# Kernel optimization log

Measured on AMD Instinct MI355X. Metric: run time of the kernel, lower is better.

## Reference

```python
import jax, jax.numpy as jnp
import numpy as np

B, C, F = 262144, 64, 256
N_ITERS = 8


def setup_inputs() -> dict:
    key = jax.random.key(0)
    ks = jax.random.split(key, 8)
    s = lambda fan_in: 1.0 / np.sqrt(fan_in)
    return {
        "y": jax.random.normal(ks[0], (B, C), jnp.float32),
        "log_det_jacobians": jnp.zeros((B,), jnp.float32),
        "v": jax.random.normal(ks[1], (B, 1, C), jnp.float32),
        "W1": jax.random.normal(ks[2], (F, C), jnp.float32) * s(C),
        "b1": jnp.zeros((F,), jnp.float32),
        "W2": jax.random.normal(ks[3], (F, F), jnp.float32) * s(F),
        "b2": jnp.zeros((F,), jnp.float32),
        "W3": jax.random.normal(ks[4], (C, F), jnp.float32) * s(F),
        "b3": jnp.zeros((C,), jnp.float32),
    }


def reference(y, log_det_jacobians, v, W1, b1, W2, b2, W3, b3):
    def mlp(t):
        h = jax.nn.elu(t)
        h = jax.nn.elu(h @ W1.T + b1)
        h = jax.nn.elu(h @ W2.T + b2)
        return h @ W3.T + b3  # [B, C]

    g_y, vjp_fn = jax.vjp(mlp, y)
    v0 = v[:, 0, :]  # n_samples = 1
    w = v0
    log_det = jnp.zeros((y.shape[0],), y.dtype)
    for k in range(1, N_ITERS + 1):
        w = vjp_fn(w)[0]              # w <- w @ J, J = dg/dy
        inner = jnp.einsum('bd,bd->b', w, v0)
        # torch code: add when (k+1) % 2 == 0 (k odd), subtract when k even
        log_det = log_det + (inner / k if (k + 1) % 2 == 0 else -inner / k)

    z = y + g_y
    return z, log_det_jacobians + log_det
```

## Files before the change

### kernel.cpp

```cpp
#include <hip/hip_runtime.h>

#define BN 262144

typedef short bf16x8 __attribute__((ext_vector_type(8)));
typedef float f32x4 __attribute__((ext_vector_type(4)));

#define MFMA16(a,b,c) __builtin_amdgcn_mfma_f32_16x16x32_bf16((a),(b),(c),0,0,0)

__device__ __forceinline__ unsigned short f2bf(float f) {
  union { float f; unsigned int u; } x; x.f = f;
  unsigned int u = x.u + 0x7fffu + ((x.u >> 16) & 1u);
  return (unsigned short)(u >> 16);
}
__device__ __forceinline__ float bf2f(unsigned int h) {
  union { unsigned int u; float f; } x; x.u = h << 16;
  return x.f;
}
__device__ __forceinline__ unsigned short tbf(float f) {
  union { float f; unsigned int u; } x; x.f = f;
  return (unsigned short)(x.u >> 16);
}

#define O_R1 0
#define O_R2 16384
#define O_R3 81920
#define O_R4 98304
#define O_R5 114688
#define O_R6 180224
#define N_WS 196608

__global__ void invres_prep(const float* __restrict__ W1, const float* __restrict__ W2,
                            const float* __restrict__ W3, unsigned short* __restrict__ wsb) {
  int idx = blockIdx.x * 256 + threadIdx.x;
  if (idx >= N_WS) return;
  int j = idx & 7;
  int lane = (idx >> 3) & 63;
  int nn = lane & 15, kn = (lane >> 4) * 8 + j;
  float val;
  if (idx < O_R2) {
    int g = idx >> 9; int s = g & 1; int ct = g >> 1;
    val = W1[(ct * 16 + nn) * 64 + (s * 32 + kn)];
  } else if (idx < O_R3) {
    int g = (idx - O_R2) >> 9; int s = g & 7; int ct = g >> 3;
    val = W2[(ct * 16 + nn) * 256 + (s * 32 + kn)];
  } else if (idx < O_R4) {
    int g = (idx - O_R3) >> 9; int s = g & 7; int ct = g >> 3;
    val = W3[(ct * 16 + nn) * 256 + (s * 32 + kn)];
  } else if (idx < O_R5) {
    int g = (idx - O_R4) >> 9; int s = g & 1; int ct = g >> 1;
    val = W3[(s * 32 + kn) * 256 + (ct * 16 + nn)];
  } else if (idx < O_R6) {
    int g = (idx - O_R5) >> 9; int s = g & 7; int ct = g >> 3;
    val = W2[(s * 32 + kn) * 256 + (ct * 16 + nn)];
  } else {
    int g = (idx - O_R6) >> 9; int s = g & 7; int ct = g >> 3;
    val = W1[(s * 32 + kn) * 64 + (ct * 16 + nn)];
  }
  wsb[idx] = f2bf(val);
}

#define L_PB  16384
#define L_WB  32768
#define L_LDP 36864
#define L_SIZE 37376

__global__ void __launch_bounds__(512, 4)
invres_main(const float* __restrict__ y, const float* __restrict__ ldj,
            const float* __restrict__ v, const float* __restrict__ b1,
            const float* __restrict__ b2, const float* __restrict__ b3,
            const unsigned short* __restrict__ wsb, float* __restrict__ out) {
  extern __shared__ char smem[];
  char* PA = smem;
  char* PB = smem + L_PB;
  char* WB = smem + L_WB;
  float* ldp = (float*)(smem + L_LDP);

  const int tid = threadIdx.x;
  const int lane = tid & 63;
  const int wid = tid >> 6;
  const int l15 = lane & 15, g16 = lane >> 4;
  const int ct0 = wid * 2;
  const int mh = wid >> 2;
  const int ctn = wid & 3;
  const int r0 = blockIdx.x * 32;

  const bf16x8* R1 = (const bf16x8*)(wsb + O_R1);
  const bf16x8* R2 = (const bf16x8*)(wsb + O_R2);
  const bf16x8* R3 = (const bf16x8*)(wsb + O_R3);
  const bf16x8* R4 = (const bf16x8*)(wsb + O_R4);
  const bf16x8* R5 = (const bf16x8*)(wsb + O_R5);
  const bf16x8* R6 = (const bf16x8*)(wsb + O_R6);

  auto ldsA = [&](const char* buf, int mm, int s) -> bf16x8 {
    int row = mm * 16 + l15;
    unsigned byte = ((unsigned)(s * 64 + g16 * 16)) ^ ((unsigned)(row & 7) << 4);
    return *(const bf16x8*)(buf + row * 512 + byte);
  };
  auto dstoreW = [&](char* buf, int mm, int cc, int r, float val) {
    int row = mm * 16 + g16 * 4 + r;
    int col = (ct0 + cc) * 16 + l15;
    *(unsigned short*)(buf + row * 512 + (((unsigned)(col * 2)) ^ ((unsigned)(row & 7) << 4))) = tbf(val);
  };
  auto gA = [&](const float* p, int mm, int s, bool elu) -> bf16x8 {
    const float* q = p + (size_t)(r0 + mm * 16 + l15) * 64 + s * 32 + g16 * 8;
    f32x4 a = __builtin_nontemporal_load((const f32x4*)q);
    f32x4 b = __builtin_nontemporal_load((const f32x4*)(q + 4));
    float xv[8] = {a[0], a[1], a[2], a[3], b[0], b[1], b[2], b[3]};
    bf16x8 f;
#pragma unroll
    for (int i = 0; i < 8; i++) {
      float x = xv[i];
      if (elu) x = x > 0.f ? x : (__expf(x) - 1.f);
      f[i] = (short)f2bf(x);
    }
    return f;
  };

  float bb1[2], bb2[2];
#pragma unroll
  for (int cc = 0; cc < 2; cc++) {
    bb1[cc] = b1[(ct0 + cc) * 16 + l15];
    bb2[cc] = b2[(ct0 + cc) * 16 + l15];
  }
  const float bb3 = b3[ctn * 16 + l15];

  unsigned d1p[8], d2p[8], d0p[2], v0p[2];
  float ldacc[4] = {0.f, 0.f, 0.f, 0.f};

  {
    f32x4 acc[2][2] = {};
#pragma unroll
    for (int s = 0; s < 2; s++) {
      bf16x8 a0 = gA(y, 0, s, true);
      bf16x8 a1 = gA(y, 1, s, true);
#pragma unroll
      for (int cc = 0; cc < 2; cc++) {
        bf16x8 B = R1[((ct0 + cc) * 2 + s) * 64 + lane];
        acc[0][cc] = MFMA16(a0, B, acc[0][cc]);
        acc[1][cc] = MFMA16(a1, B, acc[1][cc]);
      }
    }
#pragma unroll
    for (int mm = 0; mm < 2; mm++)
#pragma unroll
      for (int cc = 0; cc < 2; cc++)
#pragma unroll
        for (int r = 0; r < 4; r++) {
          float a = acc[mm][cc][r] + bb1[cc];
          float e = __expf(a);
          float h = a > 0.f ? a : (e - 1.f);
          unsigned dd = f2bf(a > 0.f ? 1.f : e);
          dstoreW(PA, mm, cc, r, h);
          int idx = (mm * 2 + cc) * 2 + (r >> 1);
          d1p[idx] = (r & 1) ? (d1p[idx] | (dd << 16)) : dd;
        }
  }
  __syncthreads();

  {
    f32x4 acc[2][2] = {};
#pragma unroll 1
    for (int s = 0; s < 8; s++) {
      bf16x8 a0 = ldsA(PA, 0, s);
      bf16x8 a1 = ldsA(PA, 1, s);
#pragma unroll
      for (int cc = 0; cc < 2; cc++) {
        bf16x8 B = R2[((ct0 + cc) * 8 + s) * 64 + lane];
        acc[0][cc] = MFMA16(a0, B, acc[0][cc]);
        acc[1][cc] = MFMA16(a1, B, acc[1][cc]);
      }
    }
#pragma unroll
    for (int mm = 0; mm < 2; mm++)
#pragma unroll
      for (int cc = 0; cc < 2; cc++)
#pragma unroll
        for (int r = 0; r < 4; r++) {
          float a = acc[mm][cc][r] + bb2[cc];
          float e = __expf(a);
          float h = a > 0.f ? a : (e - 1.f);
          unsigned dd = f2bf(a > 0.f ? 1.f : e);
          dstoreW(PB, mm, cc, r, h);
          int idx = (mm * 2 + cc) * 2 + (r >> 1);
          d2p[idx] = (r & 1) ? (d2p[idx] | (dd << 16)) : dd;
        }
  }
  __syncthreads();

  {
    f32x4 acc = {};
#pragma unroll 1
    for (int s = 0; s < 8; s++)
      acc = MFMA16(ldsA(PB, mh, s), R3[(ctn * 8 + s) * 64 + lane], acc);
#pragma unroll
    for (int r = 0; r < 4; r++) {
      int row = r0 + mh * 16 + g16 * 4 + r;
      int col = ctn * 16 + l15;
      size_t off = (size_t)row * 64 + col;
      float yv = __builtin_nontemporal_load(y + off);
      __builtin_nontemporal_store(yv + acc[r] + bb3, out + off);
      unsigned dd = f2bf(yv > 0.f ? 1.f : __expf(yv));
      unsigned vv = f2bf(__builtin_nontemporal_load(v + off));
      d0p[r >> 1] = (r & 1) ? (d0p[r >> 1] | (dd << 16)) : dd;
      v0p[r >> 1] = (r & 1) ? (v0p[r >> 1] | (vv << 16)) : vv;
    }
  }

  {
    f32x4 acc[2][2] = {};
#pragma unroll
    for (int s = 0; s < 2; s++) {
      bf16x8 a0 = gA(v, 0, s, false);
      bf16x8 a1 = gA(v, 1, s, false);
#pragma unroll
      for (int cc = 0; cc < 2; cc++) {
        bf16x8 B = R4[((ct0 + cc) * 2 + s) * 64 + lane];
        acc[0][cc] = MFMA16(a0, B, acc[0][cc]);
        acc[1][cc] = MFMA16(a1, B, acc[1][cc]);
      }
    }
#pragma unroll
    for (int mm = 0; mm < 2; mm++)
#pragma unroll
      for (int cc = 0; cc < 2; cc++)
#pragma unroll
        for (int r = 0; r < 4; r++) {
          int idx = (mm * 2 + cc) * 2 + (r >> 1);
          float u = acc[mm][cc][r] * bf2f((d2p[idx] >> ((r & 1) * 16)) & 0xffffu);
          dstoreW(PA, mm, cc, r, u);
        }
  }
  __syncthreads();

  for (int k = 1; k <= 8; ++k) {
    {
      f32x4 acc[2][2] = {};
#pragma unroll 1
      for (int s = 0; s < 8; s++) {
        bf16x8 a0 = ldsA(PA, 0, s);
        bf16x8 a1 = ldsA(PA, 1, s);
#pragma unroll
        for (int cc = 0; cc < 2; cc++) {
          bf16x8 B = R5[((ct0 + cc) * 8 + s) * 64 + lane];
          acc[0][cc] = MFMA16(a0, B, acc[0][cc]);
          acc[1][cc] = MFMA16(a1, B, acc[1][cc]);
        }
      }
#pragma unroll
      for (int mm = 0; mm < 2; mm++)
#pragma unroll
        for (int cc = 0; cc < 2; cc++)
#pragma unroll
          for (int r = 0; r < 4; r++) {
            int idx = (mm * 2 + cc) * 2 + (r >> 1);
            float u = acc[mm][cc][r] * bf2f((d1p[idx] >> ((r & 1) * 16)) & 0xffffu);
            dstoreW(PB, mm, cc, r, u);
          }
    }
    __syncthreads();

    {
      float coef = (k & 1) ? (1.f / (float)k) : (-1.f / (float)k);
      f32x4 acc = {};
#pragma unroll 1
      for (int s = 0; s < 8; s++)
        acc = MFMA16(ldsA(PB, mh, s), R6[(ctn * 8 + s) * 64 + lane], acc);
#pragma unroll
      for (int r = 0; r < 4; r++) {
        float wv = acc[r] * bf2f((d0p[r >> 1] >> ((r & 1) * 16)) & 0xffffu);
        ldacc[r] += coef * wv * bf2f((v0p[r >> 1] >> ((r & 1) * 16)) & 0xffffu);
        if (k < 8) {
          int row = mh * 16 + g16 * 4 + r;
          int col = ctn * 16 + l15;
          *(unsigned short*)(WB + row * 128 + (((unsigned)(col * 2)) ^ ((unsigned)(row & 7) << 4))) = tbf(wv);
        }
      }
    }
    if (k < 8) {
      __syncthreads();
      f32x4 acc[2][2] = {};
#pragma unroll
      for (int s = 0; s < 2; s++) {
        bf16x8 a0, a1;
#pragma unroll
        for (int mm = 0; mm < 2; mm++) {
          int row = mm * 16 + l15;
          unsigned byte = ((unsigned)(s * 64 + g16 * 16)) ^ ((unsigned)(row & 7) << 4);
          bf16x8 a = *(const bf16x8*)(WB + row * 128 + byte);
          if (mm == 0) a0 = a; else a1 = a;
        }
#pragma unroll
        for (int cc = 0; cc < 2; cc++) {
          bf16x8 B = R4[((ct0 + cc) * 2 + s) * 64 + lane];
          acc[0][cc] = MFMA16(a0, B, acc[0][cc]);
          acc[1][cc] = MFMA16(a1, B, acc[1][cc]);
        }
      }
#pragma unroll
      for (int mm = 0; mm < 2; mm++)
#pragma unroll
        for (int cc = 0; cc < 2; cc++)
#pragma unroll
          for (int r = 0; r < 4; r++) {
            int idx = (mm * 2 + cc) * 2 + (r >> 1);
            float u = acc[mm][cc][r] * bf2f((d2p[idx] >> ((r & 1) * 16)) & 0xffffu);
            dstoreW(PA, mm, cc, r, u);
          }
      __syncthreads();
    }
  }

#pragma unroll
  for (int r = 0; r < 4; r++) {
    float s = ldacc[r];
    s += __shfl_xor(s, 1);
    s += __shfl_xor(s, 2);
    s += __shfl_xor(s, 4);
    s += __shfl_xor(s, 8);
    ldacc[r] = s;
  }
  if (l15 == 0) {
#pragma unroll
    for (int r = 0; r < 4; r++) {
      int row = mh * 16 + g16 * 4 + r;
      ldp[row * 4 + ctn] = ldacc[r];
    }
  }
  __syncthreads();
  if (tid < 32) {
    float s = ldp[tid * 4] + ldp[tid * 4 + 1] + ldp[tid * 4 + 2] + ldp[tid * 4 + 3];
    int gb = r0 + tid;
    __builtin_nontemporal_store(ldj[gb] + s, out + (size_t)BN * 64 + gb);
  }
}

extern "C" void kernel_launch(void* const* d_in, const int* in_sizes, int n_in,
                              void* d_out, int out_size, void* d_ws, size_t ws_size,
                              hipStream_t stream) {
  const float* y   = (const float*)d_in[0];
  const float* ldj = (const float*)d_in[1];
  const float* v   = (const float*)d_in[2];
  const float* W1  = (const float*)d_in[3];
  const float* b1  = (const float*)d_in[4];
  const float* W2  = (const float*)d_in[5];
  const float* b2  = (const float*)d_in[6];
  const float* W3  = (const float*)d_in[7];
  const float* b3  = (const float*)d_in[8];
  unsigned short* wsb = (unsigned short*)d_ws;
  float* out = (float*)d_out;

  (void)hipFuncSetAttribute(reinterpret_cast<const void*>(&invres_main),
                            hipFuncAttributeMaxDynamicSharedMemorySize, L_SIZE);

  invres_prep<<<N_WS / 256, 256, 0, stream>>>(W1, W2, W3, wsb);
  invres_main<<<BN / 32, 512, L_SIZE, stream>>>(y, ldj, v, b1, b2, b3, wsb, out);
}
```

Before: 841.7 us.

## Double rows per block to reuse each weight fragment across four M-tiles

Each block now processes 64 batch rows instead of 32, so every wave applies each B weight fragment loaded from global/L2 to four 16-row tiles instead of two. This halves weight fetches per row and doubles MFMA work per load. In exchange, LDS per block roughly doubles to about 74 KB and register pressure rises from larger accumulator and derivative arrays, which may lower occupancy below the launch-bounds target of 4 blocks per CU.

```diff
diff --git a/kernel.cpp b/kernel.cpp
--- a/kernel.cpp
+++ b/kernel.cpp
@@ -59,10 +59,10 @@
   wsb[idx] = f2bf(val);
 }
 
-#define L_PB  16384
-#define L_WB  32768
-#define L_LDP 36864
-#define L_SIZE 37376
+#define L_PB  32768
+#define L_WB  65536
+#define L_LDP 73728
+#define L_SIZE 74752
 
 __global__ void __launch_bounds__(512, 4)
 invres_main(const float* __restrict__ y, const float* __restrict__ ldj,
@@ -80,9 +80,9 @@
   const int wid = tid >> 6;
   const int l15 = lane & 15, g16 = lane >> 4;
   const int ct0 = wid * 2;
-  const int mh = wid >> 2;
+  const int mq = (wid >> 2) * 2;
   const int ctn = wid & 3;
-  const int r0 = blockIdx.x * 32;
+  const int r0 = blockIdx.x * 64;
 
   const bf16x8* R1 = (const bf16x8*)(wsb + O_R1);
   const bf16x8* R2 = (const bf16x8*)(wsb + O_R2);
@@ -124,24 +124,26 @@
   }
   const float bb3 = b3[ctn * 16 + l15];
 
-  unsigned d1p[8], d2p[8], d0p[2], v0p[2];
-  float ldacc[4] = {0.f, 0.f, 0.f, 0.f};
+  unsigned d1p[16], d2p[16], d0p[4], v0p[4];
+  float ldacc[8];
+#pragma unroll
+  for (int i = 0; i < 8; i++) ldacc[i] = 0.f;
 
   {
-    f32x4 acc[2][2] = {};
+    f32x4 acc[4][2] = {};
 #pragma unroll
     for (int s = 0; s < 2; s++) {
-      bf16x8 a0 = gA(y, 0, s, true);
-      bf16x8 a1 = gA(y, 1, s, true);
-#pragma unroll
-      for (int cc = 0; cc < 2; cc++) {
-        bf16x8 B = R1[((ct0 + cc) * 2 + s) * 64 + lane];
-        acc[0][cc] = MFMA16(a0, B, acc[0][cc]);
-        acc[1][cc] = MFMA16(a1, B, acc[1][cc]);
-      }
-    }
-#pragma unroll
-    for (int mm = 0; mm < 2; mm++)
+      bf16x8 B0 = R1[(ct0 * 2 + s) * 64 + lane];
+      bf16x8 B1 = R1[((ct0 + 1) * 2 + s) * 64 + lane];
+#pragma unroll
+      for (int mm = 0; mm < 4; mm++) {
+        bf16x8 a = gA(y, mm, s, true);
+        acc[mm][0] = MFMA16(a, B0, acc[mm][0]);
+        acc[mm][1] = MFMA16(a, B1, acc[mm][1]);
+      }
+    }
+#pragma unroll
+    for (int mm = 0; mm < 4; mm++)
 #pragma unroll
       for (int cc = 0; cc < 2; cc++)
 #pragma unroll
@@ -158,20 +160,20 @@
   __syncthreads();
 
   {
-    f32x4 acc[2][2] = {};
+    f32x4 acc[4][2] = {};
 #pragma unroll 1
     for (int s = 0; s < 8; s++) {
-      bf16x8 a0 = ldsA(PA, 0, s);
-      bf16x8 a1 = ldsA(PA, 1, s);
-#pragma unroll
-      for (int cc = 0; cc < 2; cc++) {
-        bf16x8 B = R2[((ct0 + cc) * 8 + s) * 64 + lane];
-        acc[0][cc] = MFMA16(a0, B, acc[0][cc]);
-        acc[1][cc] = MFMA16(a1, B, acc[1][cc]);
-      }
-    }
-#pragma unroll
-    for (int mm = 0; mm < 2; mm++)
+      bf16x8 B0 = R2[(ct0 * 8 + s) * 64 + lane];
+      bf16x8 B1 = R2[((ct0 + 1) * 8 + s) * 64 + lane];
+#pragma unroll
+      for (int mm = 0; mm < 4; mm++) {
+        bf16x8 a = ldsA(PA, mm, s);
+        acc[mm][0] = MFMA16(a, B0, acc[mm][0]);
+        acc[mm][1] = MFMA16(a, B1, acc[mm][1]);
+      }
+    }
+#pragma unroll
+    for (int mm = 0; mm < 4; mm++)
 #pragma unroll
       for (int cc = 0; cc < 2; cc++)
 #pragma unroll
@@ -188,39 +190,45 @@
   __syncthreads();
 
   {
-    f32x4 acc = {};
+    f32x4 acc[2] = {};
 #pragma unroll 1
-    for (int s = 0; s < 8; s++)
-      acc = MFMA16(ldsA(PB, mh, s), R3[(ctn * 8 + s) * 64 + lane], acc);
-#pragma unroll
-    for (int r = 0; r < 4; r++) {
-      int row = r0 + mh * 16 + g16 * 4 + r;
-      int col = ctn * 16 + l15;
-      size_t off = (size_t)row * 64 + col;
-      float yv = __builtin_nontemporal_load(y + off);
-      __builtin_nontemporal_store(yv + acc[r] + bb3, out + off);
-      unsigned dd = f2bf(yv > 0.f ? 1.f : __expf(yv));
-      unsigned vv = f2bf(__builtin_nontemporal_load(v + off));
-      d0p[r >> 1] = (r & 1) ? (d0p[r >> 1] | (dd << 16)) : dd;
-      v0p[r >> 1] = (r & 1) ? (v0p[r >> 1] | (vv << 16)) : vv;
-    }
+    for (int s = 0; s < 8; s++) {
+      bf16x8 B = R3[(ctn * 8 + s) * 64 + lane];
+      acc[0] = MFMA16(ldsA(PB, mq, s), B, acc[0]);
+      acc[1] = MFMA16(ldsA(PB, mq + 1, s), B, acc[1]);
+    }
+#pragma unroll
+    for (int q = 0; q < 2; q++)
+#pragma unroll
+      for (int r = 0; r < 4; r++) {
+        int row = r0 + (mq + q) * 16 + g16 * 4 + r;
+        int col = ctn * 16 + l15;
+        size_t off = (size_t)row * 64 + col;
+        float yv = __builtin_nontemporal_load(y + off);
+        __builtin_nontemporal_store(yv + acc[q][r] + bb3, out + off);
+        unsigned dd = f2bf(yv > 0.f ? 1.f : __expf(yv));
+        unsigned vv = f2bf(__builtin_nontemporal_load(v + off));
+        int idx = q * 2 + (r >> 1);
+        d0p[idx] = (r & 1) ? (d0p[idx] | (dd << 16)) : dd;
+        v0p[idx] = (r & 1) ? (v0p[idx] | (vv << 16)) : vv;
+      }
   }
 
   {
-    f32x4 acc[2][2] = {};
+    f32x4 acc[4][2] = {};
 #pragma unroll
     for (int s = 0; s < 2; s++) {
-      bf16x8 a0 = gA(v, 0, s, false);
-      bf16x8 a1 = gA(v, 1, s, false);
-#pragma unroll
-      for (int cc = 0; cc < 2; cc++) {
-        bf16x8 B = R4[((ct0 + cc) * 2 + s) * 64 + lane];
-        acc[0][cc] = MFMA16(a0, B, acc[0][cc]);
-        acc[1][cc] = MFMA16(a1, B, acc[1][cc]);
-      }
-    }
-#pragma unroll
-    for (int mm = 0; mm < 2; mm++)
+      bf16x8 B0 = R4[(ct0 * 2 + s) * 64 + lane];
+      bf16x8 B1 = R4[((ct0 + 1) * 2 + s) * 64 + lane];
+#pragma unroll
+      for (int mm = 0; mm < 4; mm++) {
+        bf16x8 a = gA(v, mm, s, false);
+        acc[mm][0] = MFMA16(a, B0, acc[mm][0]);
+        acc[mm][1] = MFMA16(a, B1, acc[mm][1]);
+      }
+    }
+#pragma unroll
+    for (int mm = 0; mm < 4; mm++)
 #pragma unroll
       for (int cc = 0; cc < 2; cc++)
 #pragma unroll
@@ -234,20 +242,20 @@
 
   for (int k = 1; k <= 8; ++k) {
     {
-      f32x4 acc[2][2] = {};
+      f32x4 acc[4][2] = {};
 #pragma unroll 1
       for (int s = 0; s < 8; s++) {
-        bf16x8 a0 = ldsA(PA, 0, s);
-        bf16x8 a1 = ldsA(PA, 1, s);
-#pragma unroll
-        for (int cc = 0; cc < 2; cc++) {
-          bf16x8 B = R5[((ct0 + cc) * 8 + s) * 64 + lane];
-          acc[0][cc] = MFMA16(a0, B, acc[0][cc]);
-          acc[1][cc] = MFMA16(a1, B, acc[1][cc]);
-        }
-      }
-#pragma unroll
-      for (int mm = 0; mm < 2; mm++)
+        bf16x8 B0 = R5[(ct0 * 8 + s) * 64 + lane];
+        bf16x8 B1 = R5[((ct0 + 1) * 8 + s) * 64 + lane];
+#pragma unroll
+        for (int mm = 0; mm < 4; mm++) {
+          bf16x8 a = ldsA(PA, mm, s);
+          acc[mm][0] = MFMA16(a, B0, acc[mm][0]);
+          acc[mm][1] = MFMA16(a, B1, acc[mm][1]);
+        }
+      }
+#pragma unroll
+      for (int mm = 0; mm < 4; mm++)
 #pragma unroll
         for (int cc = 0; cc < 2; cc++)
 #pragma unroll
@@ -261,43 +269,45 @@
 
     {
       float coef = (k & 1) ? (1.f / (float)k) : (-1.f / (float)k);
-      f32x4 acc = {};
+      f32x4 acc[2] = {};
 #pragma unroll 1
-      for (int s = 0; s < 8; s++)
-        acc = MFMA16(ldsA(PB, mh, s), R6[(ctn * 8 + s) * 64 + lane], acc);
-#pragma unroll
-      for (int r = 0; r < 4; r++) {
-        float wv = acc[r] * bf2f((d0p[r >> 1] >> ((r & 1) * 16)) & 0xffffu);
-        ldacc[r] += coef * wv * bf2f((v0p[r >> 1] >> ((r & 1) * 16)) & 0xffffu);
-        if (k < 8) {
-          int row = mh * 16 + g16 * 4 + r;
-          int col = ctn * 16 + l15;
-          *(unsigned short*)(WB + row * 128 + (((unsigned)(col * 2)) ^ ((unsigned)(row & 7) << 4))) = tbf(wv);
-        }
-      }
+      for (int s = 0; s < 8; s++) {
+        bf16x8 B = R6[(ctn * 8 + s) * 64 + lane];
+        acc[0] = MFMA16(ldsA(PB, mq, s), B, acc[0]);
+        acc[1] = MFMA16(ldsA(PB, mq + 1, s), B, acc[1]);
+      }
+#pragma unroll
+      for (int q = 0; q < 2; q++)
+#pragma unroll
+        for (int r = 0; r < 4; r++) {
+          int idx = q * 2 + (r >> 1);
+          float wv = acc[q][r] * bf2f((d0p[idx] >> ((r & 1) * 16)) & 0xffffu);
+          ldacc[q * 4 + r] += coef * wv * bf2f((v0p[idx] >> ((r & 1) * 16)) & 0xffffu);
+          if (k < 8) {
+            int row = (mq + q) * 16 + g16 * 4 + r;
+            int col = ctn * 16 + l15;
+            *(unsigned short*)(WB + row * 128 + (((unsigned)(col * 2)) ^ ((unsigned)(row & 7) << 4))) = tbf(wv);
+          }
+        }
     }
     if (k < 8) {
       __syncthreads();
-      f32x4 acc[2][2] = {};
+      f32x4 acc[4][2] = {};
 #pragma unroll
       for (int s = 0; s < 2; s++) {
-        bf16x8 a0, a1;
-#pragma unroll
-        for (int mm = 0; mm < 2; mm++) {
+        bf16x8 B0 = R4[(ct0 * 2 + s) * 64 + lane];
+        bf16x8 B1 = R4[((ct0 + 1) * 2 + s) * 64 + lane];
+#pragma unroll
+        for (int mm = 0; mm < 4; mm++) {
           int row = mm * 16 + l15;
           unsigned byte = ((unsigned)(s * 64 + g16 * 16)) ^ ((unsigned)(row & 7) << 4);
           bf16x8 a = *(const bf16x8*)(WB + row * 128 + byte);
-          if (mm == 0) a0 = a; else a1 = a;
-        }
-#pragma unroll
-        for (int cc = 0; cc < 2; cc++) {
-          bf16x8 B = R4[((ct0 + cc) * 2 + s) * 64 + lane];
-          acc[0][cc] = MFMA16(a0, B, acc[0][cc]);
-          acc[1][cc] = MFMA16(a1, B, acc[1][cc]);
-        }
-      }
-#pragma unroll
-      for (int mm = 0; mm < 2; mm++)
+          acc[mm][0] = MFMA16(a, B0, acc[mm][0]);
+          acc[mm][1] = MFMA16(a, B1, acc[mm][1]);
+        }
+      }
+#pragma unroll
+      for (int mm = 0; mm < 4; mm++)
 #pragma unroll
         for (int cc = 0; cc < 2; cc++)
 #pragma unroll
@@ -311,23 +321,25 @@
   }
 
 #pragma unroll
-  for (int r = 0; r < 4; r++) {
-    float s = ldacc[r];
+  for (int i = 0; i < 8; i++) {
+    float s = ldacc[i];
     s += __shfl_xor(s, 1);
     s += __shfl_xor(s, 2);
     s += __shfl_xor(s, 4);
     s += __shfl_xor(s, 8);
-    ldacc[r] = s;
+    ldacc[i] = s;
   }
   if (l15 == 0) {
 #pragma unroll
-    for (int r = 0; r < 4; r++) {
-      int row = mh * 16 + g16 * 4 + r;
-      ldp[row * 4 + ctn] = ldacc[r];
-    }
+    for (int q = 0; q < 2; q++)
+#pragma unroll
+      for (int r = 0; r < 4; r++) {
+        int row = (mq + q) * 16 + g16 * 4 + r;
+        ldp[row * 4 + ctn] = ldacc[q * 4 + r];
+      }
   }
   __syncthreads();
-  if (tid < 32) {
+  if (tid < 64) {
     float s = ldp[tid * 4] + ldp[tid * 4 + 1] + ldp[tid * 4 + 2] + ldp[tid * 4 + 3];
     int gb = r0 + tid;
     __builtin_nontemporal_store(ldj[gb] + s, out + (size_t)BN * 64 + gb);
@@ -353,5 +365,5 @@
                             hipFuncAttributeMaxDynamicSharedMemorySize, L_SIZE);
 
   invres_prep<<<N_WS / 256, 256, 0, stream>>>(W1, W2, W3, wsb);
-  invres_main<<<BN / 32, 512, L_SIZE, stream>>>(y, ldj, v, b1, b2, b3, wsb, out);
-}
+  invres_main<<<BN / 64, 512, L_SIZE, stream>>>(y, ldj, v, b1, b2, b3, wsb, out);
+}
```

After: 2.003 ms. 2.38x slower.
